# Optimization experiments

Measured on AMD Instinct MI355X. Metric: run time of the kernel, lower is better.

## Reference

```python
import jax, jax.numpy as jnp
import numpy as np
import math

EARTH_RADIUS_KM = 6371.0
D_MAX_KM = 200.0
K_D = 64

B, N, D, R = 64, 128, 128, 4096


def setup_inputs() -> dict:
    key = jax.random.key(0)
    ks = jax.random.split(key, 7)
    S = jax.random.normal(ks[0], (B, N, D), dtype=jnp.float32)
    region_emb = jax.random.normal(ks[1], (R, D), dtype=jnp.float32)
    traj_lat = jax.random.uniform(ks[2], (B, N), dtype=jnp.float32)
    traj_lon = jax.random.uniform(ks[3], (B, N), dtype=jnp.float32)
    region_centroids = jax.random.uniform(ks[4], (R, 2), dtype=jnp.float32)
    key_padding_mask = jax.random.randint(ks[5], (B, N), 0, 2).astype(bool)
    E_d_match = jax.random.normal(ks[6], (K_D,), dtype=jnp.float32) * 0.1
    return {"S": S, "region_emb": region_emb, "traj_lat": traj_lat,
            "traj_lon": traj_lon, "region_centroids": region_centroids,
            "key_padding_mask": key_padding_mask, "E_d_match": E_d_match}


def _haversine_km(lat1, lon1, lat2, lon2):
    deg2rad = math.pi / 180.0
    lat1r = lat1 * deg2rad
    lat2r = lat2 * deg2rad
    dlat = (lat2 - lat1) * deg2rad
    dlon = (lon2 - lon1) * deg2rad
    a = jnp.sin(dlat / 2) ** 2 + jnp.cos(lat1r) * jnp.cos(lat2r) * jnp.sin(dlon / 2) ** 2
    a = jnp.clip(a, 0.0, 1.0)
    return EARTH_RADIUS_KM * 2.0 * jnp.arcsin(jnp.sqrt(a))


def _interp_scalar(table, x):
    K = table.shape[0]
    x = jnp.clip(x, 0.0, K - 1 - 1e-06)
    k = jnp.floor(x).astype(jnp.int32)
    frac = x - k.astype(x.dtype)
    lo = table[k]
    hi = table[jnp.minimum(k + 1, K - 1)]
    return (1.0 - frac) * lo + frac * hi


def reference(S, region_emb, traj_lat, traj_lon, region_centroids,
              key_padding_mask, E_d_match):
    Dm = S.shape[-1]
    cand_lat = region_centroids[:, 0]  # [R]
    cand_lon = region_centroids[:, 1]
    # [B, n, R] pairwise distance trajectory-position <-> region centroid
    dd = _haversine_km(traj_lat[:, :, None], traj_lon[:, :, None],
                       cand_lat[None, None, :], cand_lon[None, None, :])
    d_bin = jnp.clip(dd, 0.0, D_MAX_KM) / D_MAX_KM * (K_D - 1)
    bias_match = _interp_scalar(E_d_match, d_bin)  # [B, n, R]
    scores = jnp.einsum('bnd,rd->bnr', S, region_emb) / math.sqrt(Dm)
    scores = scores + bias_match
    mask = key_padding_mask[:, :, None]  # [B, n, 1]
    scores = jnp.where(mask, -jnp.inf, scores)
    attn = jnp.nan_to_num(jax.nn.softmax(scores, axis=1), nan=0.0)
    scores_safe = jnp.where(mask, 0.0, scores)
    return (attn * scores_safe).sum(axis=1)  # [B, R]
```

## Files before the change

kernel.cpp:

```cpp
#include <hip/hip_runtime.h>
#include <math.h>

#define BB 64
#define NN 128
#define DD 128
#define RR 4096
#define KD 64

typedef _Float16 f16x8 __attribute__((ext_vector_type(8)));
typedef float    float4v __attribute__((ext_vector_type(4)));

__global__ __launch_bounds__(256, 4)
void matching_kernel(const float* __restrict__ S,
                     const float* __restrict__ Remb,
                     const float* __restrict__ tlat,
                     const float* __restrict__ tlon,
                     const float* __restrict__ cent,
                     const int*   __restrict__ kpm,
                     const float* __restrict__ Etab,
                     float* __restrict__ out)
{
    __shared__ _Float16 ldsE[128 * 128];
    __shared__ float colLatP[128], colLonP[128], colCos[128];
    __shared__ float rowLatP[128], rowLonP[128], rowCn[128];
    __shared__ float2 tab2[KD];
    __shared__ int   idx[128];
    __shared__ unsigned long long smask[2];

    float* pe = (float*)ldsE;
    float* pw = (float*)ldsE + 512;

    const int tid = threadIdx.x;
    const int b  = blockIdx.y;
    const int r0 = blockIdx.x * 128;
    const int wv = tid >> 6, lane = tid & 63;
    const int lrow = lane & 15, quad = lane >> 4;

    const float D2R    = 0.017453292519943295f;
    const float HD2R   = 0.008726646259971648f;
    const float L2E    = 1.4426950408889634f;
    const float SCALE2 = 0.08838834764831845f * 1.4426950408889634f;
    const float XMSQ   = 4013.73f * 4013.73f;
    const float LN2    = 0.6931471805599453f;

    if (tid < 128) {
        int r = r0 + tid;
        float cla = cent[2 * r], clo = cent[2 * r + 1];
        colLatP[tid] = cla * HD2R; colLonP[tid] = clo * HD2R;
        colCos[tid]  = cosf(cla * D2R);
        bool valid = (kpm[b * NN + tid] == 0);
        unsigned long long m = __ballot(valid);
        if (lane == 0) smask[wv] = m;
    } else if (tid < 128 + KD) {
        int k = tid - 128;
        float lo = Etab[k];
        float hi = Etab[k < KD - 1 ? k + 1 : KD - 1];
        tab2[k] = make_float2(lo * L2E, (hi - lo) * L2E);
    }
    const float* gE = Remb + (size_t)r0 * DD;
    for (int i = tid; i < 128 * 16; i += 256) {
        int row = i >> 4, c = i & 15;
        const float* p = &gE[row * DD + c * 8];
        float4 lo = *(const float4*)p, hi = *(const float4*)(p + 4);
        f16x8 h;
        h[0] = (_Float16)lo.x; h[1] = (_Float16)lo.y;
        h[2] = (_Float16)lo.z; h[3] = (_Float16)lo.w;
        h[4] = (_Float16)hi.x; h[5] = (_Float16)hi.y;
        h[6] = (_Float16)hi.z; h[7] = (_Float16)hi.w;
        *(f16x8*)&ldsE[row * 128 + ((c ^ (row & 15)) * 8)] = h;
    }
    __syncthreads();

    const unsigned long long m0 = smask[0], m1 = smask[1];
    const int c0 = __popcll(m0);
    const int V  = c0 + __popcll(m1);
    const int Mt = (V + 15) >> 4;

    if (tid < 128) {
        unsigned long long mw = (tid < 64) ? m0 : m1;
        int ln = tid & 63;
        if ((mw >> ln) & 1ull) {
            int pos = __popcll(mw & ((1ull << ln) - 1ull)) + (tid < 64 ? 0 : c0);
            idx[pos] = tid;
        }
    }
    __syncthreads();

    if (tid < 128) {
        if (tid < V) {
            int n = idx[tid];
            float la = tlat[b * NN + n], lo = tlon[b * NN + n];
            rowLatP[tid] = la * HD2R; rowLonP[tid] = lo * HD2R;
            rowCn[tid]   = cosf(la * D2R);
        } else {
            rowLatP[tid] = 0.0f; rowLonP[tid] = 0.0f; rowCn[tid] = -1.0f;
        }
    }

    const float* gS = S + (size_t)b * NN * DD;
    const bool a1 = (wv + 4) < Mt;
    f16x8 afrag[2][4];
#pragma unroll
    for (int i = 0; i < 2; ++i) {
        int tile = wv + 4 * i;
        if (tile < Mt) {
            int rc = tile * 16 + lrow;
            int n  = idx[rc < V ? rc : V - 1];
            const float* rp = &gS[n * DD];
#pragma unroll
            for (int kk = 0; kk < 4; ++kk) {
                float4 lo = *(const float4*)&rp[kk * 32 + quad * 8];
                float4 hi = *(const float4*)&rp[kk * 32 + quad * 8 + 4];
                f16x8 a;
                a[0] = (_Float16)lo.x; a[1] = (_Float16)lo.y;
                a[2] = (_Float16)lo.z; a[3] = (_Float16)lo.w;
                a[4] = (_Float16)hi.x; a[5] = (_Float16)hi.y;
                a[6] = (_Float16)hi.z; a[7] = (_Float16)hi.w;
                afrag[i][kk] = a;
            }
        }
    }

    float4v acc[2][8] = {};
    if (wv < Mt) {
#pragma unroll
        for (int kk = 0; kk < 4; ++kk) {
#pragma unroll
            for (int tr = 0; tr < 8; ++tr) {
                int c = kk * 4 + quad;
                f16x8 bb = *(const f16x8*)&ldsE[(tr * 16 + lrow) * 128 + ((c ^ lrow) * 8)];
                acc[0][tr] = __builtin_amdgcn_mfma_f32_16x16x32_f16(afrag[0][kk], bb, acc[0][tr], 0, 0, 0);
                if (a1)
                    acc[1][tr] = __builtin_amdgcn_mfma_f32_16x16x32_f16(afrag[1][kk], bb, acc[1][tr], 0, 0, 0);
            }
        }
    }
    __syncthreads();

    float tlP[8], toP[8], cn8[8];
#pragma unroll
    for (int i = 0; i < 2; ++i)
#pragma unroll
        for (int e = 0; e < 4; ++e) {
            int n = (wv + 4 * i) * 16 + quad * 4 + e;
            int j = i * 4 + e;
            tlP[j] = rowLatP[n]; toP[j] = rowLonP[n]; cn8[j] = rowCn[n];
        }

#pragma unroll
    for (int tr = 0; tr < 8; ++tr) {
        int col = tr * 16 + lrow;
        float claP = colLatP[col], cloP = colLonP[col], cc = colCos[col];
        float es = 0.0f, ws2 = 0.0f;
        if (wv < Mt) {
#pragma unroll
            for (int i = 0; i < 2; ++i) {
                if (i == 1 && !a1) break;
#pragma unroll
                for (int e = 0; e < 4; ++e) {
                    int j = i * 4 + e;
                    float hd = claP - tlP[j];
                    float ho = cloP - toP[j];
                    float a  = fmaf(hd, hd, (cn8[j] * cc) * (ho * ho));
                    float x  = fminf(__builtin_amdgcn_sqrtf(a * XMSQ), 62.999996f);
                    int   k  = (int)x;
                    float fr = x - (float)k;
                    float2 te = tab2[k];
                    float bias2 = fmaf(fr, te.y, te.x);
                    float s2 = fmaf(acc[i][tr][e], SCALE2, bias2);
                    float ex = __builtin_amdgcn_exp2f(s2);
                    ex = (cn8[j] < 0.0f) ? 0.0f : ex;
                    es += ex;
                    ws2 = fmaf(ex, s2, ws2);
                }
            }
        }
        es  += __shfl_xor(es, 16, 64);  es  += __shfl_xor(es, 32, 64);
        ws2 += __shfl_xor(ws2, 16, 64); ws2 += __shfl_xor(ws2, 32, 64);
        if (lane < 16) { pe[wv * 128 + col] = es; pw[wv * 128 + col] = ws2; }
    }
    __syncthreads();

    if (tid < 128) {
        float es = pe[tid] + pe[128 + tid] + pe[256 + tid] + pe[384 + tid];
        float ws = pw[tid] + pw[128 + tid] + pw[256 + tid] + pw[384 + tid];
        float o = es > 0.0f ? (ws / es) * LN2 : 0.0f;
        out[(size_t)b * RR + r0 + tid] = o;
    }
}

extern "C" void kernel_launch(void* const* d_in, const int* in_sizes, int n_in,
                              void* d_out, int out_size, void* d_ws, size_t ws_size,
                              hipStream_t stream) {
    const float* S    = (const float*)d_in[0];
    const float* Remb = (const float*)d_in[1];
    const float* tlat = (const float*)d_in[2];
    const float* tlon = (const float*)d_in[3];
    const float* cent = (const float*)d_in[4];
    const int*   kpm  = (const int*)d_in[5];
    const float* Etab = (const float*)d_in[6];
    float* out = (float*)d_out;

    dim3 grid(RR / 128, BB, 1);
    dim3 block(256, 1, 1);
    matching_kernel<<<grid, block, 0, stream>>>(S, Remb, tlat, tlon, cent, kpm, Etab, out);
}
```

Before: 96.26 us.

## Pre-convert inputs to fp16 in a separate kernel and stream K-chunks through LDS

Adds a conversion kernel that writes fp16 copies of region embeddings and S to workspace. The main kernel reads these fp16 copies instead of converting fp32 per block. It uses 64-region tiles with a double-buffered 32-wide K-chunk pipeline in LDS, shrinking LDS use and raising the occupancy hint to 5. The distance scaling constant is folded into the coordinates to drop a multiply. This halves global bytes per tile but adds an extra launch and a full workspace round-trip, and doubles the grid, so geometry and row setup are redone more often.

```diff
diff --git a/kernel.cpp b/kernel.cpp
--- a/kernel.cpp
+++ b/kernel.cpp
@@ -8,11 +8,31 @@
 #define KD 64
 
 typedef _Float16 f16x8 __attribute__((ext_vector_type(8)));
+typedef _Float16 f16x4 __attribute__((ext_vector_type(4)));
 typedef float    float4v __attribute__((ext_vector_type(4)));
 
-__global__ __launch_bounds__(256, 4)
-void matching_kernel(const float* __restrict__ S,
-                     const float* __restrict__ Remb,
+#define WS_S_OFF (RR * DD)
+
+__global__ __launch_bounds__(256)
+void convert_kernel(const float* __restrict__ S, const float* __restrict__ E,
+                    _Float16* __restrict__ ws) {
+    int i = blockIdx.x * 256 + threadIdx.x;
+    const int NE4 = (RR * DD) / 4;
+    if (i < NE4) {
+        float4 v = ((const float4*)E)[i];
+        f16x4 h = {(_Float16)v.x, (_Float16)v.y, (_Float16)v.z, (_Float16)v.w};
+        ((f16x4*)ws)[i] = h;
+    } else {
+        int j = i - NE4;
+        float4 v = ((const float4*)S)[j];
+        f16x4 h = {(_Float16)v.x, (_Float16)v.y, (_Float16)v.z, (_Float16)v.w};
+        ((f16x4*)(ws + WS_S_OFF))[j] = h;
+    }
+}
+
+__global__ __launch_bounds__(256, 5)
+void matching_kernel(const _Float16* __restrict__ wsE,
+                     const _Float16* __restrict__ wsS,
                      const float* __restrict__ tlat,
                      const float* __restrict__ tlon,
                      const float* __restrict__ cent,
@@ -20,34 +40,31 @@
                      const float* __restrict__ Etab,
                      float* __restrict__ out)
 {
-    __shared__ _Float16 ldsE[128 * 128];
-    __shared__ float colLatP[128], colLonP[128], colCos[128];
-    __shared__ float rowLatP[128], rowLonP[128], rowCn[128];
+    __shared__ _Float16 ldsB[2][64 * 32];
+    __shared__ float colLatX[64], colLonX[64], colCos[64];
+    __shared__ float rowLatX[128], rowLonX[128], rowCn[128];
     __shared__ float2 tab2[KD];
     __shared__ int   idx[128];
     __shared__ unsigned long long smask[2];
-
-    float* pe = (float*)ldsE;
-    float* pw = (float*)ldsE + 512;
+    __shared__ float pe[4][64], pw[4][64];
 
     const int tid = threadIdx.x;
     const int b  = blockIdx.y;
-    const int r0 = blockIdx.x * 128;
+    const int r0 = blockIdx.x * 64;
     const int wv = tid >> 6, lane = tid & 63;
     const int lrow = lane & 15, quad = lane >> 4;
 
     const float D2R    = 0.017453292519943295f;
-    const float HD2R   = 0.008726646259971648f;
+    const float HSC    = 0.008726646259971648f * 4013.73f;
     const float L2E    = 1.4426950408889634f;
     const float SCALE2 = 0.08838834764831845f * 1.4426950408889634f;
-    const float XMSQ   = 4013.73f * 4013.73f;
     const float LN2    = 0.6931471805599453f;
 
+    const int srow = tid >> 2, scth = tid & 3;
+    const _Float16* gB = wsE + (size_t)(r0 + srow) * DD + scth * 8;
+    uint4 creg = *(const uint4*)gB;
+
     if (tid < 128) {
-        int r = r0 + tid;
-        float cla = cent[2 * r], clo = cent[2 * r + 1];
-        colLatP[tid] = cla * HD2R; colLonP[tid] = clo * HD2R;
-        colCos[tid]  = cosf(cla * D2R);
         bool valid = (kpm[b * NN + tid] == 0);
         unsigned long long m = __ballot(valid);
         if (lane == 0) smask[wv] = m;
@@ -56,18 +73,11 @@
         float lo = Etab[k];
         float hi = Etab[k < KD - 1 ? k + 1 : KD - 1];
         tab2[k] = make_float2(lo * L2E, (hi - lo) * L2E);
-    }
-    const float* gE = Remb + (size_t)r0 * DD;
-    for (int i = tid; i < 128 * 16; i += 256) {
-        int row = i >> 4, c = i & 15;
-        const float* p = &gE[row * DD + c * 8];
-        float4 lo = *(const float4*)p, hi = *(const float4*)(p + 4);
-        f16x8 h;
-        h[0] = (_Float16)lo.x; h[1] = (_Float16)lo.y;
-        h[2] = (_Float16)lo.z; h[3] = (_Float16)lo.w;
-        h[4] = (_Float16)hi.x; h[5] = (_Float16)hi.y;
-        h[6] = (_Float16)hi.z; h[7] = (_Float16)hi.w;
-        *(f16x8*)&ldsE[row * 128 + ((c ^ (row & 15)) * 8)] = h;
+    } else {
+        int c = tid - 192, r = r0 + c;
+        float cla = cent[2 * r], clo = cent[2 * r + 1];
+        colLatX[c] = cla * HSC; colLonX[c] = clo * HSC;
+        colCos[c]  = cosf(cla * D2R);
     }
     __syncthreads();
 
@@ -90,100 +100,80 @@
         if (tid < V) {
             int n = idx[tid];
             float la = tlat[b * NN + n], lo = tlon[b * NN + n];
-            rowLatP[tid] = la * HD2R; rowLonP[tid] = lo * HD2R;
+            rowLatX[tid] = la * HSC; rowLonX[tid] = lo * HSC;
             rowCn[tid]   = cosf(la * D2R);
-        } else {
-            rowLatP[tid] = 0.0f; rowLonP[tid] = 0.0f; rowCn[tid] = -1.0f;
-        }
-    }
-
-    const float* gS = S + (size_t)b * NN * DD;
-    const bool a1 = (wv + 4) < Mt;
-    f16x8 afrag[2][4];
-#pragma unroll
-    for (int i = 0; i < 2; ++i) {
-        int tile = wv + 4 * i;
-        if (tile < Mt) {
-            int rc = tile * 16 + lrow;
-            int n  = idx[rc < V ? rc : V - 1];
-            const float* rp = &gS[n * DD];
-#pragma unroll
-            for (int kk = 0; kk < 4; ++kk) {
-                float4 lo = *(const float4*)&rp[kk * 32 + quad * 8];
-                float4 hi = *(const float4*)&rp[kk * 32 + quad * 8 + 4];
-                f16x8 a;
-                a[0] = (_Float16)lo.x; a[1] = (_Float16)lo.y;
-                a[2] = (_Float16)lo.z; a[3] = (_Float16)lo.w;
-                a[4] = (_Float16)hi.x; a[5] = (_Float16)hi.y;
-                a[6] = (_Float16)hi.z; a[7] = (_Float16)hi.w;
-                afrag[i][kk] = a;
-            }
-        }
-    }
-
-    float4v acc[2][8] = {};
-    if (wv < Mt) {
-#pragma unroll
-        for (int kk = 0; kk < 4; ++kk) {
-#pragma unroll
-            for (int tr = 0; tr < 8; ++tr) {
-                int c = kk * 4 + quad;
-                f16x8 bb = *(const f16x8*)&ldsE[(tr * 16 + lrow) * 128 + ((c ^ lrow) * 8)];
-                acc[0][tr] = __builtin_amdgcn_mfma_f32_16x16x32_f16(afrag[0][kk], bb, acc[0][tr], 0, 0, 0);
-                if (a1)
-                    acc[1][tr] = __builtin_amdgcn_mfma_f32_16x16x32_f16(afrag[1][kk], bb, acc[1][tr], 0, 0, 0);
-            }
-        }
-    }
-    __syncthreads();
-
-    float tlP[8], toP[8], cn8[8];
+        } else { rowLatX[tid] = 0.0f; rowLonX[tid] = 0.0f; rowCn[tid] = -1.0f; }
+    }
+
+    const bool t0a = (wv < Mt), t1a = (wv + 4) < Mt;
+    int rc0 = wv * 16 + lrow, rc1 = (wv + 4) * 16 + lrow;
+    const _Float16* pA0 = wsS + (size_t)(b * NN + idx[(rc0 < V ? rc0 : V - 1)]) * DD;
+    const _Float16* pA1 = wsS + (size_t)(b * NN + idx[(rc1 < V ? rc1 : V - 1)]) * DD;
+
+    float4v acc[2][4] = {};
+    const int sslot = (scth ^ (srow & 3)) * 8;
+#pragma unroll
+    for (int kk = 0; kk < 4; ++kk) {
+        *(uint4*)&ldsB[kk & 1][srow * 32 + sslot] = creg;
+        if (kk < 3) creg = *(const uint4*)(gB + (kk + 1) * 32);
+        f16x8 af0, af1;
+        if (t0a) af0 = *(const f16x8*)(pA0 + kk * 32 + quad * 8);
+        if (t1a) af1 = *(const f16x8*)(pA1 + kk * 32 + quad * 8);
+        __syncthreads();
+#pragma unroll
+        for (int tr = 0; tr < 4; ++tr) {
+            int row = tr * 16 + lrow;
+            f16x8 bb = *(const f16x8*)&ldsB[kk & 1][row * 32 + ((quad ^ (row & 3)) * 8)];
+            if (t0a) acc[0][tr] = __builtin_amdgcn_mfma_f32_16x16x32_f16(af0, bb, acc[0][tr], 0, 0, 0);
+            if (t1a) acc[1][tr] = __builtin_amdgcn_mfma_f32_16x16x32_f16(af1, bb, acc[1][tr], 0, 0, 0);
+        }
+    }
+
+    float tlX[8], toX[8], cn8[8];
 #pragma unroll
     for (int i = 0; i < 2; ++i)
 #pragma unroll
         for (int e = 0; e < 4; ++e) {
             int n = (wv + 4 * i) * 16 + quad * 4 + e;
             int j = i * 4 + e;
-            tlP[j] = rowLatP[n]; toP[j] = rowLonP[n]; cn8[j] = rowCn[n];
-        }
-
-#pragma unroll
-    for (int tr = 0; tr < 8; ++tr) {
+            tlX[j] = rowLatX[n]; toX[j] = rowLonX[n]; cn8[j] = rowCn[n];
+        }
+
+#pragma unroll
+    for (int tr = 0; tr < 4; ++tr) {
         int col = tr * 16 + lrow;
-        float claP = colLatP[col], cloP = colLonP[col], cc = colCos[col];
+        float claX = colLatX[col], cloX = colLonX[col], cc = colCos[col];
         float es = 0.0f, ws2 = 0.0f;
-        if (wv < Mt) {
-#pragma unroll
-            for (int i = 0; i < 2; ++i) {
-                if (i == 1 && !a1) break;
-#pragma unroll
-                for (int e = 0; e < 4; ++e) {
-                    int j = i * 4 + e;
-                    float hd = claP - tlP[j];
-                    float ho = cloP - toP[j];
-                    float a  = fmaf(hd, hd, (cn8[j] * cc) * (ho * ho));
-                    float x  = fminf(__builtin_amdgcn_sqrtf(a * XMSQ), 62.999996f);
-                    int   k  = (int)x;
-                    float fr = x - (float)k;
-                    float2 te = tab2[k];
-                    float bias2 = fmaf(fr, te.y, te.x);
-                    float s2 = fmaf(acc[i][tr][e], SCALE2, bias2);
-                    float ex = __builtin_amdgcn_exp2f(s2);
-                    ex = (cn8[j] < 0.0f) ? 0.0f : ex;
-                    es += ex;
-                    ws2 = fmaf(ex, s2, ws2);
-                }
+#pragma unroll
+        for (int i = 0; i < 2; ++i) {
+            if (i == 0 ? !t0a : !t1a) continue;
+#pragma unroll
+            for (int e = 0; e < 4; ++e) {
+                int j = i * 4 + e;
+                float hd = claX - tlX[j];
+                float ho = cloX - toX[j];
+                float a  = fmaf(hd, hd, (cn8[j] * cc) * (ho * ho));
+                float x  = fminf(__builtin_amdgcn_sqrtf(a), 62.999996f);
+                int   k  = (int)x;
+                float fr = x - (float)k;
+                float2 te = tab2[k];
+                float bias2 = fmaf(fr, te.y, te.x);
+                float s2 = fmaf(acc[i][tr][e], SCALE2, bias2);
+                float ex = __builtin_amdgcn_exp2f(s2);
+                ex = (cn8[j] < 0.0f) ? 0.0f : ex;
+                es += ex;
+                ws2 = fmaf(ex, s2, ws2);
             }
         }
         es  += __shfl_xor(es, 16, 64);  es  += __shfl_xor(es, 32, 64);
         ws2 += __shfl_xor(ws2, 16, 64); ws2 += __shfl_xor(ws2, 32, 64);
-        if (lane < 16) { pe[wv * 128 + col] = es; pw[wv * 128 + col] = ws2; }
+        if (lane < 16) { pe[wv][col] = es; pw[wv][col] = ws2; }
     }
     __syncthreads();
 
-    if (tid < 128) {
-        float es = pe[tid] + pe[128 + tid] + pe[256 + tid] + pe[384 + tid];
-        float ws = pw[tid] + pw[128 + tid] + pw[256 + tid] + pw[384 + tid];
+    if (tid < 64) {
+        float es = pe[0][tid] + pe[1][tid] + pe[2][tid] + pe[3][tid];
+        float ws = pw[0][tid] + pw[1][tid] + pw[2][tid] + pw[3][tid];
         float o = es > 0.0f ? (ws / es) * LN2 : 0.0f;
         out[(size_t)b * RR + r0 + tid] = o;
     }
@@ -200,8 +190,11 @@
     const int*   kpm  = (const int*)d_in[5];
     const float* Etab = (const float*)d_in[6];
     float* out = (float*)d_out;
-
-    dim3 grid(RR / 128, BB, 1);
-    dim3 block(256, 1, 1);
-    matching_kernel<<<grid, block, 0, stream>>>(S, Remb, tlat, tlon, cent, kpm, Etab, out);
+    _Float16* ws = (_Float16*)d_ws;
+
+    convert_kernel<<<1536, 256, 0, stream>>>(S, Remb, ws);
+
+    dim3 grid(RR / 64, BB, 1);
+    matching_kernel<<<grid, dim3(256, 1, 1), 0, stream>>>(
+        ws, ws + WS_S_OFF, tlat, tlon, cent, kpm, Etab, out);
 }
```

After: 89.99 us. 6.5% less time.
